# Kernel optimization log

Hardware: AMD Instinct MI355X
Metric: run time of the kernel (lower is better)

The kernel has to match this reference:

```python
import jax, jax.numpy as jnp
import numpy as np
from jax import lax

D_MODEL = 512
D_STATE = 32
D_CONV = 4
D_INNER = 2 * D_MODEL
DT_RANK = (D_MODEL + 15) // 16  # 32
B_SZ, L = 8, 1024
EPS = 1e-12


def _mamba_params(key, pfx):
    ks = jax.random.split(key, 6)
    s = 0.02
    p = {}
    p[pfx + '_in_w'] = jax.random.normal(ks[0], (2 * D_INNER, D_MODEL)) * s
    p[pfx + '_conv_w'] = jax.random.normal(ks[1], (D_INNER, D_CONV)) * s
    p[pfx + '_conv_b'] = jnp.zeros((D_INNER,))
    p[pfx + '_xproj_w'] = jax.random.normal(ks[2], (DT_RANK + 2 * D_STATE, D_INNER)) * s
    p[pfx + '_dt_w'] = jax.random.normal(ks[3], (D_INNER, DT_RANK)) * s
    p[pfx + '_dt_b'] = jax.random.uniform(ks[4], (D_INNER,), minval=-4.0, maxval=-2.0)
    p[pfx + '_A_log'] = jnp.log(jnp.broadcast_to(jnp.arange(1, D_STATE + 1, dtype=jnp.float32), (D_INNER, D_STATE)))
    p[pfx + '_D'] = jnp.ones((D_INNER,))
    p[pfx + '_out_w'] = jax.random.normal(ks[5], (D_MODEL, D_INNER)) * s
    return p


def setup_inputs() -> dict:
    key = jax.random.key(0)
    ks = jax.random.split(key, 10)
    inp = {
        'hidden_states': jax.random.normal(ks[0], (B_SZ, L, D_MODEL)),
        'lengths': jax.random.randint(ks[1], (B_SZ,), 1, L + 1, dtype=jnp.int32),
    }
    inp.update(_mamba_params(ks[2], 'f'))
    inp.update(_mamba_params(ks[3], 'b'))
    s = 0.02
    inp['proj_w'] = jax.random.normal(ks[4], (1, 2)) * 0.5 + 0.5
    inp['proj_b'] = jnp.zeros((1,))
    inp['ln_g'] = jnp.ones((D_MODEL,))
    inp['ln_b'] = jnp.zeros((D_MODEL,))
    inp['ffn_w1'] = jax.random.normal(ks[5], (4 * D_MODEL, D_MODEL)) * s
    inp['ffn_b1'] = jnp.zeros((4 * D_MODEL,))
    inp['ffn_w2'] = jax.random.normal(ks[6], (D_MODEL, 4 * D_MODEL)) * s
    inp['ffn_b2'] = jnp.zeros((D_MODEL,))
    inp['ffn_ln_g'] = jnp.ones((D_MODEL,))
    inp['ffn_ln_b'] = jnp.zeros((D_MODEL,))
    return inp


def _layernorm(x, g, b):
    mu = jnp.mean(x, -1, keepdims=True)
    var = jnp.mean(jnp.square(x - mu), -1, keepdims=True)
    return (x - mu) * lax.rsqrt(var + EPS) * g + b


def _selective_scan(delta, Bm, Cm, u, A, D):
    # delta,u: (B,L,Di); Bm,Cm: (B,L,N); A: (Di,N); D: (Di,)
    def step(h, inp):
        d_t, B_t, C_t, u_t = inp
        dA = jnp.exp(d_t[..., None] * A)                 # (B,Di,N)
        h = dA * h + (d_t * u_t)[..., None] * B_t[:, None, :]
        y = jnp.einsum('bdn,bn->bd', h, C_t)
        return h, y
    h0 = jnp.zeros((u.shape[0], A.shape[0], A.shape[1]), u.dtype)
    xs = (delta.transpose(1, 0, 2), Bm.transpose(1, 0, 2),
          Cm.transpose(1, 0, 2), u.transpose(1, 0, 2))
    _, ys = lax.scan(step, h0, xs)
    return ys.transpose(1, 0, 2) + u * D


def _mamba(x, in_w, conv_w, conv_b, xproj_w, dt_w, dt_b, A_log, Dp, out_w):
    xz = jnp.einsum('bld,ed->ble', x, in_w)              # (B,L,2Di)
    x_in, z = jnp.split(xz, 2, axis=-1)
    # causal depthwise conv1d
    xc = jnp.pad(x_in.transpose(0, 2, 1), ((0, 0), (0, 0), (D_CONV - 1, 0)))
    xc = lax.conv_general_dilated(xc, conv_w[:, None, :], (1,), 'VALID',
                                  dimension_numbers=('NCH', 'OIH', 'NCH'),
                                  feature_group_count=D_INNER)
    xc = jax.nn.silu(xc + conv_b[None, :, None]).transpose(0, 2, 1)  # (B,L,Di)
    x_dbl = jnp.einsum('bld,ed->ble', xc, xproj_w)
    dt, Bm, Cm = jnp.split(x_dbl, [DT_RANK, DT_RANK + D_STATE], axis=-1)
    delta = jax.nn.softplus(jnp.einsum('blr,dr->bld', dt, dt_w) + dt_b)
    A = -jnp.exp(A_log)
    y = _selective_scan(delta, Bm, Cm, xc, A, Dp)
    y = y * jax.nn.silu(z)
    return jnp.einsum('bld,ed->ble', y, out_w)


def reference(hidden_states, lengths,
              f_in_w, f_conv_w, f_conv_b, f_xproj_w, f_dt_w, f_dt_b, f_A_log, f_D, f_out_w,
              b_in_w, b_conv_w, b_conv_b, b_xproj_w, b_dt_w, b_dt_b, b_A_log, b_D, b_out_w,
              proj_w, proj_b, ln_g, ln_b,
              ffn_w1, ffn_b1, ffn_w2, ffn_b2, ffn_ln_g, ffn_ln_b):
    x = hidden_states
    hf = _mamba(x, f_in_w, f_conv_w, f_conv_b, f_xproj_w, f_dt_w, f_dt_b, f_A_log, f_D, f_out_w)
    hb = _mamba(jnp.flip(x, 1), b_in_w, b_conv_w, b_conv_b, b_xproj_w, b_dt_w, b_dt_b, b_A_log, b_D, b_out_w)
    hb = jnp.flip(hb, 1)
    # Linear(2,1) over stacked [hf,hb] on last axis
    out = hf * proj_w[0, 0] + hb * proj_w[0, 1] + proj_b[0]
    out1 = _layernorm(out + x, ln_g, ln_b)  # dropout = identity (eval)
    h = jax.nn.gelu(jnp.einsum('bld,ed->ble', out1, ffn_w1) + ffn_b1, approximate=False)
    h = jnp.einsum('ble,de->bld', h, ffn_w2) + ffn_b2
    return _layernorm(h + out1, ffn_ln_g, ffn_ln_b)
```

## Files before the change

### kernel.cpp

```cpp
#include <hip/hip_runtime.h>
#include <hip/hip_bf16.h>
#include <hip/hip_fp16.h>
#include <math.h>

typedef __hip_bfloat16 bf16;
typedef __attribute__((ext_vector_type(8))) short bfrag;
typedef __attribute__((ext_vector_type(4))) float ffrag;
typedef __attribute__((ext_vector_type(4))) float f4;
typedef __attribute__((ext_vector_type(4))) short sh4;

#define BSZ    8
#define LSEQ   1024
#define DMODEL 512
#define DINNER 1024
#define DSTATE 32
#define DTRANK 32
#define MROWS  (BSZ * LSEQ)

__device__ __forceinline__ float bf2f(bf16 v) { return __bfloat162float(v); }
__device__ __forceinline__ float s2f(short s) {
    union { unsigned u; float f; } c; c.u = ((unsigned)(unsigned short)s) << 16; return c.f;
}
__device__ __forceinline__ short f2s(float v) {
    union { bf16 b; short s; } u; u.b = __float2bfloat16(v); return u.s;
}
__device__ __forceinline__ void stC(float* p, size_t i, float v) { p[i] = v; }
__device__ __forceinline__ void stC(bf16* p, size_t i, float v) { p[i] = __float2bfloat16(v); }
__device__ __forceinline__ float fsigmoid(float x) {
    return __builtin_amdgcn_rcpf(1.f + __expf(-x));
}
__device__ __forceinline__ float fexp2(float x) { return __builtin_amdgcn_exp2f(x); }

__device__ __forceinline__ float dload(const void* p, size_t i, int f) {
    if (f == 1) return ((const float*)p)[i];
    if (f == 2) return __half2float(((const __half*)p)[i]);
    if (f == 3) return (float)((const double*)p)[i];
    return bf2f(((const bf16*)p)[i]);
}

enum { ACT_NONE = 0, ACT_SOFTPLUS = 1, ACT_GELU = 2 };

__global__ void resolve_kernel(const void* a8, const void* d9, const void* d22,
                               const void* s0, const void* s1, int* flags)
{
    if (blockIdx.x != 0) return;
    const int lane = threadIdx.x;
    const int cand[4] = {1, 0, 2, 3};
    int fw = -1;
    for (int ci = 0; ci < 4 && fw < 0; ++ci) {
        int f = cand[ci];
        bool ok = true;
        if (lane < 48) {
            float e = logf((float)((lane & 31) + 1));
            float v = dload(a8, lane, f);
            ok = (v == v) && fabsf(v - e) <= 0.02f * e + 0.02f;
        } else if (lane < 56) {
            int k = lane - 48;
            ok = fabsf(dload(d9, k, f) - 1.f) <= 0.01f &&
                 fabsf(dload(d22, k, f) - 1.f) <= 0.01f;
        }
        if (__all(ok)) fw = f;
    }
    int fx = -1, xs = -1;
    for (int si = 0; si < 2 && fx < 0; ++si) {
        const void* p = (si == 0) ? s0 : s1;
        for (int ci = 0; ci < 4 && fx < 0; ++ci) {
            int f = cand[ci];
            bool ok = true;
            float s = 0.f, s2 = 0.f;
            for (int k = lane; k < 256; k += 64) {
                float v = dload(p, k, f);
                ok = ok && (v == v) && fabsf(v) < 16.f;
                s += v; s2 += v * v;
            }
            int allok = __all(ok);
            for (int m = 1; m < 64; m <<= 1) {
                s += __shfl_xor(s, m); s2 += __shfl_xor(s2, m);
            }
            if (allok) {
                float mu = s * (1.f / 256.f);
                float var = s2 * (1.f / 256.f) - mu * mu;
                if (var > 0.25f && var < 4.f) { fx = f; xs = si; }
            }
        }
    }
    if (lane == 0) {
        flags[0] = (fw < 0) ? 1 : fw;
        flags[1] = (fx < 0) ? 1 : fx;
        flags[2] = (xs < 0) ? 0 : xs;
        flags[3] = (fw == 1 && fx == 1) ? 1 : 0;
    }
}

__global__ __launch_bounds__(256) void cvt_x_kernel(const void* x0, const void* x1,
                                                    bf16* __restrict__ dst,
                                                    const int* __restrict__ flags)
{
    const void* x = flags[2] ? x1 : x0;
    const int fx = flags[1];
    int i = blockIdx.x * 256 + threadIdx.x;
    if (fx == 1) {
        f4 v = ((const f4*)x)[i];
        sh4 o;
#pragma unroll
        for (int j = 0; j < 4; ++j) o[j] = f2s(v[j]);
        ((sh4*)dst)[i] = o;
    } else {
#pragma unroll
        for (int j = 0; j < 4; ++j)
            dst[(size_t)i * 4 + j] = __float2bfloat16(dload(x, (size_t)i * 4 + j, fx));
    }
}

__global__ __launch_bounds__(256) void cvt3_kernel(
    const float* __restrict__ s0, bf16* __restrict__ d0, int n0,
    const float* __restrict__ s1, bf16* __restrict__ d1, int n1,
    const float* __restrict__ s2, bf16* __restrict__ d2, int n2)
{
    int i = blockIdx.x * 256 + threadIdx.x;
    const float* s; bf16* d; int off;
    if (i < n0) { s = s0; d = d0; off = i; }
    else if (i < n0 + n1) { s = s1; d = d1; off = i - n0; }
    else if (i < n0 + n1 + n2) { s = s2; d = d2; off = i - n0 - n1; }
    else return;
    f4 v = ((const f4*)s)[off];
    sh4 o;
#pragma unroll
    for (int j = 0; j < 4; ++j) o[j] = f2s(v[j]);
    ((sh4*)d)[off] = o;
}

__global__ __launch_bounds__(256) void transpose_kernel(
    const bf16* __restrict__ src, bf16* __restrict__ dst, int R, int D)
{
    __shared__ short t[64][72];
    const int r0 = blockIdx.x * 64, d0 = blockIdx.y * 64;
    const int tr = threadIdx.x >> 3;
    const int tc = (threadIdx.x & 7) * 8;
#pragma unroll
    for (int h = 0; h < 2; ++h) {
        int d = tr + h * 32;
        bfrag v = *(const bfrag*)&src[(size_t)(d0 + d) * R + r0 + tc];
#pragma unroll
        for (int j = 0; j < 8; ++j) t[tc + j][d] = v[j];
    }
    __syncthreads();
#pragma unroll
    for (int h = 0; h < 2; ++h) {
        int r = tr + h * 32;
        bfrag v = *(const bfrag*)&t[r][tc];
        *(bfrag*)&dst[(size_t)(r0 + r) * D + d0 + tc] = v;
    }
}

__global__ __launch_bounds__(256) void transpose_f32_kernel(
    const float* __restrict__ src, float* __restrict__ dst, int R)
{
    __shared__ float t[64][68];
    const int m0 = blockIdx.x * 64;
    const int tr = threadIdx.x >> 2;
    const int tc = (threadIdx.x & 3) * 16;
#pragma unroll
    for (int j = 0; j < 4; ++j) {
        f4 v = *(const f4*)&src[(size_t)tr * R + m0 + tc + j * 4];
#pragma unroll
        for (int e = 0; e < 4; ++e) t[tc + j * 4 + e][tr] = v[e];
    }
    __syncthreads();
#pragma unroll
    for (int j = 0; j < 4; ++j) {
        f4 v = *(const f4*)&t[tr][tc + j * 4];
        *(f4*)&dst[(size_t)(m0 + tr) * 64 + tc + j * 4] = v;
    }
}

__device__ __forceinline__ void glds16(const bf16* g, short* l)
{
    __builtin_amdgcn_global_load_lds(
        (const __attribute__((address_space(1))) void*)g,
        (__attribute__((address_space(3))) void*)l,
        16, 0, 0);
}

template <int FLIPB, int ACT, typename CT>
__global__ __launch_bounds__(256) void bgemm_kernel(
    const bf16* __restrict__ A, int lda,
    const bf16* __restrict__ B, int ldb,
    const float* __restrict__ bias,
    CT* __restrict__ C, int ldc, int K)
{
    __shared__ __align__(16) short As[2][128 * 32];
    __shared__ __align__(16) short Bs[2][128 * 32];
    const int tid = threadIdx.x;
    const int bm = blockIdx.y * 128, bn = blockIdx.x * 128;
    const int lane = tid & 63, w = tid >> 6;

    const int srow = lane >> 2;
    const int skc  = (lane & 3) << 3;
    const int arow0 = bm + w * 32 + srow;
    int brow0 = bn + w * 32 + srow;
    int brow1 = brow0 + 16;
    if (FLIPB) {
        brow0 = (brow0 & ~(LSEQ - 1)) + (LSEQ - 1 - (brow0 & (LSEQ - 1)));
        brow1 = (brow1 & ~(LSEQ - 1)) + (LSEQ - 1 - (brow1 & (LSEQ - 1)));
    }
    const bf16* ga0 = A + (size_t)arow0 * lda + skc;
    const bf16* ga1 = ga0 + (size_t)16 * lda;
    const bf16* gb0 = B + (size_t)brow0 * ldb + skc;
    const bf16* gb1 = B + (size_t)brow1 * ldb + skc;
    const int lA0 = (w * 32) * 32, lA1 = (w * 32 + 16) * 32;

    const int wm = (w & 1) << 6, wn = (w >> 1) << 6;
    const int lm = lane & 15, quad = lane >> 4;

    ffrag acc[4][4];
#pragma unroll
    for (int i = 0; i < 4; ++i)
#pragma unroll
        for (int j = 0; j < 4; ++j)
#pragma unroll
            for (int e = 0; e < 4; ++e) acc[i][j][e] = 0.f;

    glds16(ga0, &As[0][lA0]);
    glds16(ga1, &As[0][lA1]);
    glds16(gb0, &Bs[0][lA0]);
    glds16(gb1, &Bs[0][lA1]);
    __syncthreads();

    int cur = 0;
    for (int k0 = 0; k0 < K; k0 += 32) {
        if (k0 + 32 < K) {
            glds16(ga0 + k0 + 32, &As[cur ^ 1][lA0]);
            glds16(ga1 + k0 + 32, &As[cur ^ 1][lA1]);
            glds16(gb0 + k0 + 32, &Bs[cur ^ 1][lA0]);
            glds16(gb1 + k0 + 32, &Bs[cur ^ 1][lA1]);
        }
        bfrag af[4], bfv[4];
#pragma unroll
        for (int ti = 0; ti < 4; ++ti)
            af[ti] = *(const bfrag*)&As[cur][(wm + ti * 16 + lm) * 32 + quad * 8];
#pragma unroll
        for (int tj = 0; tj < 4; ++tj)
            bfv[tj] = *(const bfrag*)&Bs[cur][(wn + tj * 16 + lm) * 32 + quad * 8];
#pragma unroll
        for (int ti = 0; ti < 4; ++ti)
#pragma unroll
            for (int tj = 0; tj < 4; ++tj)
                acc[ti][tj] = __builtin_amdgcn_mfma_f32_16x16x32_bf16(
                    af[ti], bfv[tj], acc[ti][tj], 0, 0, 0);
        __syncthreads();
        cur ^= 1;
    }

#pragma unroll
    for (int tj = 0; tj < 4; ++tj) {
        int col = bn + wn + tj * 16 + lm;
        float bcv = bias ? bias[col] : 0.f;
#pragma unroll
        for (int ti = 0; ti < 4; ++ti) {
#pragma unroll
            for (int r2 = 0; r2 < 4; ++r2) {
                int rowg = bm + wm + ti * 16 + quad * 4 + r2;
                float v = acc[ti][tj][r2] + bcv;
                if (ACT == ACT_GELU) v = 0.5f * v * (1.f + erff(v * 0.70710678118654752f));
                stC(C, (size_t)rowg * ldc + col, v);
            }
        }
    }
}

template <int ACT, typename CT>
__global__ __launch_bounds__(256) void bgemm64_kernel(
    const bf16* __restrict__ A, int lda,
    const bf16* __restrict__ B, int ldb,
    const float* __restrict__ bias,
    CT* __restrict__ C, int ldc, int M, int K)
{
    __shared__ __align__(16) short As[2][128 * 64];
    __shared__ __align__(16) short Bs[2][64 * 64];
    const int tid = threadIdx.x;
    const int bm = blockIdx.y * 128, bn = blockIdx.x * 64;
    const int lane = tid & 63, w = tid >> 6;

    const int lr = lane >> 3;
    const int sc = ((lane & 7) ^ lr) << 3;

    const bf16* ga[4];
#pragma unroll
    for (int a = 0; a < 4; ++a) {
        int ar = bm + w * 32 + a * 8 + lr;
        if (ar >= M) ar = M - 1;
        ga[a] = A + (size_t)ar * lda + sc;
    }
    const bf16* gb[2];
#pragma unroll
    for (int a = 0; a < 2; ++a) {
        int br = bn + w * 16 + a * 8 + lr;
        gb[a] = B + (size_t)br * ldb + sc;
    }
    const int lA = (w * 32) * 64, lB = (w * 16) * 64;

    const int wm = (w & 1) << 6, wn = (w >> 1) << 5;
    const int lm = lane & 15, quad = lane >> 4;

    ffrag acc[4][2];
#pragma unroll
    for (int i = 0; i < 4; ++i)
#pragma unroll
        for (int j = 0; j < 2; ++j)
#pragma unroll
            for (int e = 0; e < 4; ++e) acc[i][j][e] = 0.f;

#pragma unroll
    for (int a = 0; a < 4; ++a) glds16(ga[a], &As[0][lA + a * 8 * 64]);
#pragma unroll
    for (int a = 0; a < 2; ++a) glds16(gb[a], &Bs[0][lB + a * 8 * 64]);
    __syncthreads();

    int cur = 0;
    for (int k0 = 0; k0 < K; k0 += 64) {
        if (k0 + 64 < K) {
#pragma unroll
            for (int a = 0; a < 4; ++a) glds16(ga[a] + k0 + 64, &As[cur ^ 1][lA + a * 8 * 64]);
#pragma unroll
            for (int a = 0; a < 2; ++a) glds16(gb[a] + k0 + 64, &Bs[cur ^ 1][lB + a * 8 * 64]);
        }
        bfrag af[2][4], bfv[2][2];
#pragma unroll
        for (int kk = 0; kk < 2; ++kk) {
#pragma unroll
            for (int ti = 0; ti < 4; ++ti) {
                int row = wm + ti * 16 + lm;
                int c = kk * 4 + quad;
                af[kk][ti] = *(const bfrag*)&As[cur][row * 64 + ((c ^ (row & 7)) << 3)];
            }
#pragma unroll
            for (int tj = 0; tj < 2; ++tj) {
                int row = wn + tj * 16 + lm;
                int c = kk * 4 + quad;
                bfv[kk][tj] = *(const bfrag*)&Bs[cur][row * 64 + ((c ^ (row & 7)) << 3)];
            }
        }
#pragma unroll
        for (int kk = 0; kk < 2; ++kk)
#pragma unroll
            for (int ti = 0; ti < 4; ++ti)
#pragma unroll
                for (int tj = 0; tj < 2; ++tj)
                    acc[ti][tj] = __builtin_amdgcn_mfma_f32_16x16x32_bf16(
                        af[kk][ti], bfv[kk][tj], acc[ti][tj], 0, 0, 0);
        __syncthreads();
        cur ^= 1;
    }

#pragma unroll
    for (int tj = 0; tj < 2; ++tj) {
        int col = bn + wn + tj * 16 + lm;
        float bcv = bias ? bias[col] : 0.f;
#pragma unroll
        for (int ti = 0; ti < 4; ++ti) {
#pragma unroll
            for (int r2 = 0; r2 < 4; ++r2) {
                int rowg = bm + wm + ti * 16 + quad * 4 + r2;
                if (rowg < M) {
                    float v = acc[ti][tj][r2] + bcv;
                    if (ACT == ACT_GELU) v = 0.5f * v * (1.f + erff(v * 0.70710678118654752f));
                    stC(C, (size_t)rowg * ldc + col, v);
                }
            }
        }
    }
}

__global__ __launch_bounds__(256) void dt_kernel(
    const float* __restrict__ xdT,
    const float* __restrict__ dt_w,
    const float* __restrict__ dt_b,
    bf16* __restrict__ delta_T)
{
    const int m = blockIdx.x * 256 + threadIdx.x;
    const int d0 = blockIdx.y * 64;
    float v[32];
#pragma unroll
    for (int r = 0; r < 32; ++r) v[r] = xdT[(size_t)r * MROWS + m];
    for (int d = d0; d < d0 + 64; ++d) {
        float acc = dt_b[d];
#pragma unroll
        for (int r = 0; r < 32; ++r) acc = fmaf(dt_w[d * 32 + r], v[r], acc);
        acc = (acc > 20.f) ? acc : log1pf(__expf(acc));
        delta_T[(size_t)d * MROWS + m] = __float2bfloat16(acc);
    }
}

__global__ __launch_bounds__(256) void conv_silu_kernel(
    const bf16* __restrict__ xin_T,
    const void* __restrict__ cw,
    const void* __restrict__ cb,
    bf16* __restrict__ u_T,
    const int* __restrict__ flags)
{
    const int fw = flags[0];
    int blk = blockIdx.x;
    int chunk = blk & 3;
    int db = blk >> 2;
    int b = db & 7;
    int d = db >> 3;
    int l = chunk * 256 + threadIdx.x;
    size_t base = (size_t)d * MROWS + b * LSEQ;
    float w0 = dload(cw, d * 4 + 0, fw), w1 = dload(cw, d * 4 + 1, fw);
    float w2 = dload(cw, d * 4 + 2, fw), w3 = dload(cw, d * 4 + 3, fw);
    float acc = dload(cb, d, fw);
    if (l >= 3) acc += bf2f(xin_T[base + l - 3]) * w0;
    if (l >= 2) acc += bf2f(xin_T[base + l - 2]) * w1;
    if (l >= 1) acc += bf2f(xin_T[base + l - 1]) * w2;
    acc += bf2f(xin_T[base + l]) * w3;
    u_T[base + l] = __float2bfloat16(acc * fsigmoid(acc));
}

#define SCH 8
struct ScanBuf { float dl[SCH], uv[SCH], Bv[SCH], Cv[SCH]; float zsc, usc; };

__device__ __forceinline__ void scan_load(ScanBuf& s,
    const bf16* __restrict__ dT, const bf16* __restrict__ uT,
    const bf16* __restrict__ zT, const float* __restrict__ xm,
    size_t lb, size_t mb, int n)
{
    bfrag dv = *(const bfrag*)&dT[lb];
    bfrag uv = *(const bfrag*)&uT[lb];
#pragma unroll
    for (int j = 0; j < SCH; ++j) { s.dl[j] = s2f(dv[j]); s.uv[j] = s2f(uv[j]); }
    s.zsc = bf2f(zT[lb + (n & 7)]);
    s.usc = bf2f(uT[lb + (n & 7)]);
#pragma unroll
    for (int j = 0; j < SCH; ++j) {
        s.Bv[j] = xm[(mb + j) * 64 + n];
        s.Cv[j] = xm[(mb + j) * 64 + 32 + n];
    }
}

__device__ __forceinline__ void scan_compute(const ScanBuf& s, float& h,
    float Ad2, float Dd, bf16* __restrict__ yT, size_t lb,
    bool b0, bool b1, bool b2, bool wr)
{
    float p[SCH];
#pragma unroll
    for (int j = 0; j < SCH; ++j) {
        float dlv = s.dl[j];
        h = fexp2(dlv * Ad2) * h + dlv * s.uv[j] * s.Bv[j];
        p[j] = h * s.Cv[j];
    }
    float q[4];
#pragma unroll
    for (int jj = 0; jj < 4; ++jj) {
        float keep = b0 ? p[2 * jj + 1] : p[2 * jj];
        float send = b0 ? p[2 * jj] : p[2 * jj + 1];
        q[jj] = keep + __shfl_xor(send, 1);
    }
    float r0 = (b1 ? q[1] : q[0]) + __shfl_xor(b1 ? q[0] : q[1], 2);
    float r1 = (b1 ? q[3] : q[2]) + __shfl_xor(b1 ? q[2] : q[3], 2);
    float t = (b2 ? r1 : r0) + __shfl_xor(b2 ? r0 : r1, 4);
    t += __shfl_xor(t, 8);
    t += __shfl_xor(t, 16);
    if (wr) {
        float y = t + s.usc * Dd;
        float g = s.zsc;
        y *= g * fsigmoid(g);
        yT[lb + (threadIdx.x & 7)] = __float2bfloat16(y);
    }
}

__global__ __launch_bounds__(256) void scan_kernel(
    const bf16* __restrict__ delta_T,
    bf16* __restrict__ u_T,
    const bf16* __restrict__ z_T,
    const float* __restrict__ xdbl_m,
    const void* __restrict__ A_log,
    const void* __restrict__ Dp,
    const int* __restrict__ flags)
{
    const int fw = flags[0];
    const int tid = threadIdx.x;
    const int n = tid & 31;
    const int dloc = tid >> 5;
    const int gd = blockIdx.x * 8 + dloc;
    const int b = gd >> 10;
    const int d = gd & (DINNER - 1);
    const bool b0 = n & 1, b1 = n & 2, b2 = n & 4;
    const bool wr = (n < 8);

    const float Ad2 = -__expf(dload(A_log, d * DSTATE + n, fw)) * 1.44269504088896341f;
    const float Dd = dload(Dp, d, fw);
    const size_t lbase = (size_t)d * MROWS + b * LSEQ;
    const size_t mbase = (size_t)b * LSEQ;
    float h = 0.f;

    ScanBuf bufA, bufB;
    scan_load(bufA, delta_T, u_T, z_T, xdbl_m, lbase, mbase, n);
    for (int c0 = 0; c0 < LSEQ / SCH; c0 += 2) {
        scan_load(bufB, delta_T, u_T, z_T, xdbl_m,
                  lbase + (size_t)(c0 + 1) * SCH, mbase + (size_t)(c0 + 1) * SCH, n);
        scan_compute(bufA, h, Ad2, Dd, u_T, lbase + (size_t)c0 * SCH, b0, b1, b2, wr);
        if (c0 + 2 < LSEQ / SCH)
            scan_load(bufA, delta_T, u_T, z_T, xdbl_m,
                      lbase + (size_t)(c0 + 2) * SCH, mbase + (size_t)(c0 + 2) * SCH, n);
        scan_compute(bufB, h, Ad2, Dd, u_T, lbase + (size_t)(c0 + 1) * SCH, b0, b1, b2, wr);
    }
}

__global__ __launch_bounds__(256) void combine_ln_kernel(
    const bf16* __restrict__ hf, const bf16* __restrict__ hb,
    const void* __restrict__ x0, const void* __restrict__ x1,
    const void* __restrict__ pw, const void* __restrict__ pb,
    const void* __restrict__ g, const void* __restrict__ be,
    bf16* __restrict__ out1,
    const int* __restrict__ flags)
{
    const int fw = flags[0];
    const int fx = flags[1];
    const void* x = flags[2] ? x1 : x0;
    int row = blockIdx.x;
    int b = row >> 10, l = row & (LSEQ - 1);
    int rrow = (b << 10) + (LSEQ - 1 - l);
    float pw0 = dload(pw, 0, fw), pw1 = dload(pw, 1, fw), pbv = dload(pb, 0, fw);
    __shared__ float red[2][4];
    float v[2], s = 0.f, s2 = 0.f;
#pragma unroll
    for (int i = 0; i < 2; ++i) {
        int c = threadIdx.x + i * 256;
        float val = bf2f(hf[(size_t)row * DMODEL + c]) * pw0
                  + bf2f(hb[(size_t)rrow * DMODEL + c]) * pw1
                  + pbv + dload(x, (size_t)row * DMODEL + c, fx);
        v[i] = val; s += val; s2 += val * val;
    }
    for (int m = 1; m < 64; m <<= 1) { s += __shfl_xor(s, m); s2 += __shfl_xor(s2, m); }
    int w = threadIdx.x >> 6;
    if ((threadIdx.x & 63) == 0) { red[0][w] = s; red[1][w] = s2; }
    __syncthreads();
    s = red[0][0] + red[0][1] + red[0][2] + red[0][3];
    s2 = red[1][0] + red[1][1] + red[1][2] + red[1][3];
    float mu = s * (1.f / DMODEL);
    float var = s2 * (1.f / DMODEL) - mu * mu;
    float r = rsqrtf(fmaxf(var, 0.f) + 1e-12f);
#pragma unroll
    for (int i = 0; i < 2; ++i) {
        int c = threadIdx.x + i * 256;
        float val = (v[i] - mu) * r * dload(g, c, fw) + dload(be, c, fw);
        out1[(size_t)row * DMODEL + c] = __float2bfloat16(val);
    }
}

__global__ __launch_bounds__(256) void final_ln_kernel(
    const float* __restrict__ out2, const bf16* __restrict__ out1,
    const void* __restrict__ g, const void* __restrict__ be,
    float* __restrict__ out,
    const int* __restrict__ flags)
{
    const int fw = flags[0];
    const int valid = flags[3];
    int row = blockIdx.x;
    __shared__ float red[2][4];
    float v[2], s = 0.f, s2 = 0.f;
#pragma unroll
    for (int i = 0; i < 2; ++i) {
        int c = threadIdx.x + i * 256;
        float val = out2[(size_t)row * DMODEL + c] + bf2f(out1[(size_t)row * DMODEL + c]);
        v[i] = val; s += val; s2 += val * val;
    }
    for (int m = 1; m < 64; m <<= 1) { s += __shfl_xor(s, m); s2 += __shfl_xor(s2, m); }
    int w = threadIdx.x >> 6;
    if ((threadIdx.x & 63) == 0) { red[0][w] = s; red[1][w] = s2; }
    __syncthreads();
    s = red[0][0] + red[0][1] + red[0][2] + red[0][3];
    s2 = red[1][0] + red[1][1] + red[1][2] + red[1][3];
    float mu = s * (1.f / DMODEL);
    float var = s2 * (1.f / DMODEL) - mu * mu;
    float r = rsqrtf(fmaxf(var, 0.f) + 1e-12f);
#pragma unroll
    for (int i = 0; i < 2; ++i) {
        int c = threadIdx.x + i * 256;
        float val = (v[i] - mu) * r * dload(g, c, fw) + dload(be, c, fw);
        out[(size_t)row * DMODEL + c] = valid ? val : 0.f;
    }
}

extern "C" void kernel_launch(void* const* d_in, const int* in_sizes, int n_in,
                              void* d_out, int out_size, void* d_ws, size_t ws_size,
                              hipStream_t stream)
{
    const void* x0 = d_in[0];
    const void* x1 = d_in[1];
    const void* proj_w   = d_in[20];
    const void* proj_b   = d_in[21];
    const void* ln_g     = d_in[22];
    const void* ln_b     = d_in[23];
    const float* ffn_w1  = (const float*)d_in[24];
    const float* ffn_b1  = (const float*)d_in[25];
    const float* ffn_w2  = (const float*)d_in[26];
    const float* ffn_b2  = (const float*)d_in[27];
    const void* ffn_ln_g = d_in[28];
    const void* ffn_ln_b = d_in[29];

    char* wsb = (char*)d_ws;
    char* ob  = (char*)d_out;
    bf16*  xin_T   = (bf16*)(wsb + 0);
    bf16*  z_T     = (bf16*)(wsb + (16u << 20));
    bf16*  uy_T    = (bf16*)(wsb + (32u << 20));
    bf16*  u_rm    = (bf16*)(wsb + 0);
    bf16*  delta_T = (bf16*)(wsb + 0);
    bf16*  y_rm    = (bf16*)(wsb + 0);
    float* xdT     = (float*)(wsb + (48u << 20));
    bf16*  in_w_bf = (bf16*)(wsb + (51u << 20));
    float* xdbl_m  = (float*)(wsb + (51u << 20));
    bf16*  xp_w_bf = (bf16*)(wsb + (53u << 20));
    bf16*  o_w_bf  = (bf16*)(wsb + (54u << 20));
    bf16*  hf      = (bf16*)d_out;
    bf16*  hb      = (bf16*)d_out + (size_t)MROWS * DMODEL;
    bf16*  xbf     = (bf16*)(ob + (8u << 20));
    bf16*  w1bf    = (bf16*)(ob + 0);
    bf16*  w2bf    = (bf16*)(ob + (2u << 20));
    bf16*  out1    = (bf16*)(wsb + 0);
    bf16*  ffn_h   = (bf16*)(wsb + (8u << 20));
    float* out2    = (float*)(wsb + (40u << 20));
    int*   flags   = (int*)(wsb + (56u << 20));

    dim3 blk(256);

    resolve_kernel<<<dim3(1), dim3(64), 0, stream>>>(
        d_in[8], d_in[9], d_in[22], x0, x1, flags);
    cvt_x_kernel<<<dim3(4096), blk, 0, stream>>>(x0, x1, xbf, flags);

    for (int dir = 0; dir < 2; ++dir) {
        int pb0 = 2 + dir * 9;
        const float* in_w    = (const float*)d_in[pb0 + 0];
        const void*  conv_w  = d_in[pb0 + 1];
        const void*  conv_b  = d_in[pb0 + 2];
        const float* xproj_w = (const float*)d_in[pb0 + 3];
        const float* dt_w    = (const float*)d_in[pb0 + 4];
        const float* dt_b    = (const float*)d_in[pb0 + 5];
        const void*  A_log   = d_in[pb0 + 6];
        const void*  Dp      = d_in[pb0 + 7];
        const float* out_w   = (const float*)d_in[pb0 + 8];
        bf16* hout = (dir == 0) ? hf : hb;

        cvt3_kernel<<<dim3(1632), blk, 0, stream>>>(
            in_w, in_w_bf, (2048 * 512) / 4,
            xproj_w, xp_w_bf, (96 * 1024) / 4,
            out_w, o_w_bf, (512 * 1024) / 4);

        if (dir == 0)
            bgemm_kernel<0, ACT_NONE, bf16><<<dim3(64, 16), blk, 0, stream>>>(
                in_w_bf, DMODEL, xbf, DMODEL, nullptr, xin_T, MROWS, DMODEL);
        else
            bgemm_kernel<1, ACT_NONE, bf16><<<dim3(64, 16), blk, 0, stream>>>(
                in_w_bf, DMODEL, xbf, DMODEL, nullptr, xin_T, MROWS, DMODEL);

        conv_silu_kernel<<<dim3(DINNER * BSZ * 4), blk, 0, stream>>>(
            xin_T, conv_w, conv_b, uy_T, flags);
        transpose_kernel<<<dim3(128, 16), blk, 0, stream>>>(uy_T, u_rm, MROWS, DINNER);
        bgemm64_kernel<ACT_NONE, float><<<dim3(128, 1), blk, 0, stream>>>(
            xp_w_bf, DINNER, u_rm, DINNER, nullptr, xdT, MROWS, 96, DINNER);
        transpose_f32_kernel<<<dim3(128), blk, 0, stream>>>(
            xdT + (size_t)32 * MROWS, xdbl_m, MROWS);
        dt_kernel<<<dim3(32, 16), blk, 0, stream>>>(xdT, dt_w, dt_b, delta_T);
        scan_kernel<<<dim3((BSZ * DINNER) / 8), blk, 0, stream>>>(
            delta_T, uy_T, z_T, xdbl_m, A_log, Dp, flags);
        transpose_kernel<<<dim3(128, 16), blk, 0, stream>>>(uy_T, y_rm, MROWS, DINNER);
        bgemm64_kernel<ACT_NONE, bf16><<<dim3(8, 64), blk, 0, stream>>>(
            y_rm, DINNER, o_w_bf, DINNER, nullptr, hout, DMODEL, MROWS, DINNER);
    }

    combine_ln_kernel<<<dim3(MROWS), blk, 0, stream>>>(
        hf, hb, x0, x1, proj_w, proj_b, ln_g, ln_b, out1, flags);
    cvt3_kernel<<<dim3(2048), blk, 0, stream>>>(
        ffn_w1, w1bf, (2048 * 512) / 4,
        ffn_w2, w2bf, (512 * 2048) / 4,
        nullptr, nullptr, 0);
    bgemm_kernel<0, ACT_GELU, bf16><<<dim3(16, 64), blk, 0, stream>>>(
        out1, DMODEL, w1bf, DMODEL, ffn_b1, ffn_h, 2048, DMODEL);
    bgemm64_kernel<ACT_NONE, float><<<dim3(8, 64), blk, 0, stream>>>(
        ffn_h, 2048, w2bf, 2048, ffn_b2, out2, DMODEL, MROWS, 2048);
    final_ln_kernel<<<dim3(MROWS), blk, 0, stream>>>(
        out2, out1, ffn_ln_g, ffn_ln_b, (float*)d_out, flags);
}
```

Before: 869.3 us.

## Fuse x_proj B/C transpose into GEMM epilogue with scan-friendly blocked layout

The x_proj GEMM epilogue now writes the dt rows as before but scatters the B and C rows directly into a blocked layout ([m/8][64][8]). This removes the separate f32 transpose kernel from each direction. The scan kernel then loads its 8 B and 8 C values per chunk as two float4 vectors each instead of 16 strided scalar loads. The cost is scattered, less coalesced stores in the GEMM epilogue.

Result: faster. 849.8 us (-2.2%).

```diff
diff --git a/kernel.cpp b/kernel.cpp
--- a/kernel.cpp
+++ b/kernel.cpp
@@ -153,27 +153,6 @@
     }
 }
 
-__global__ __launch_bounds__(256) void transpose_f32_kernel(
-    const float* __restrict__ src, float* __restrict__ dst, int R)
-{
-    __shared__ float t[64][68];
-    const int m0 = blockIdx.x * 64;
-    const int tr = threadIdx.x >> 2;
-    const int tc = (threadIdx.x & 3) * 16;
-#pragma unroll
-    for (int j = 0; j < 4; ++j) {
-        f4 v = *(const f4*)&src[(size_t)tr * R + m0 + tc + j * 4];
-#pragma unroll
-        for (int e = 0; e < 4; ++e) t[tc + j * 4 + e][tr] = v[e];
-    }
-    __syncthreads();
-#pragma unroll
-    for (int j = 0; j < 4; ++j) {
-        f4 v = *(const f4*)&t[tr][tc + j * 4];
-        *(f4*)&dst[(size_t)(m0 + tr) * 64 + tc + j * 4] = v;
-    }
-}
-
 __device__ __forceinline__ void glds16(const bf16* g, short* l)
 {
     __builtin_amdgcn_global_load_lds(
@@ -269,12 +248,14 @@
     }
 }
 
-template <int ACT, typename CT>
+template <int ACT, int XPROJ, typename CT>
 __global__ __launch_bounds__(256) void bgemm64_kernel(
     const bf16* __restrict__ A, int lda,
     const bf16* __restrict__ B, int ldb,
     const float* __restrict__ bias,
-    CT* __restrict__ C, int ldc, int M, int K)
+    CT* __restrict__ C, int ldc,
+    float* __restrict__ C2,
+    int M, int K)
 {
     __shared__ __align__(16) short As[2][128 * 64];
     __shared__ __align__(16) short Bs[2][64 * 64];
@@ -362,7 +343,13 @@
 #pragma unroll
             for (int r2 = 0; r2 < 4; ++r2) {
                 int rowg = bm + wm + ti * 16 + quad * 4 + r2;
-                if (rowg < M) {
+                if (XPROJ) {
+                    float v = acc[ti][tj][r2];
+                    if (rowg < 32)
+                        ((float*)C)[(size_t)rowg * ldc + col] = v;
+                    else if (rowg < 96)
+                        C2[(((size_t)col >> 3) * 64 + (rowg - 32)) * 8 + (col & 7)] = v;
+                } else if (rowg < M) {
                     float v = acc[ti][tj][r2] + bcv;
                     if (ACT == ACT_GELU) v = 0.5f * v * (1.f + erff(v * 0.70710678118654752f));
                     stC(C, (size_t)rowg * ldc + col, v);
@@ -423,7 +410,7 @@
 __device__ __forceinline__ void scan_load(ScanBuf& s,
     const bf16* __restrict__ dT, const bf16* __restrict__ uT,
     const bf16* __restrict__ zT, const float* __restrict__ xm,
-    size_t lb, size_t mb, int n)
+    size_t lb, int coff, int n)
 {
     bfrag dv = *(const bfrag*)&dT[lb];
     bfrag uv = *(const bfrag*)&uT[lb];
@@ -431,10 +418,16 @@
     for (int j = 0; j < SCH; ++j) { s.dl[j] = s2f(dv[j]); s.uv[j] = s2f(uv[j]); }
     s.zsc = bf2f(zT[lb + (n & 7)]);
     s.usc = bf2f(uT[lb + (n & 7)]);
-#pragma unroll
-    for (int j = 0; j < SCH; ++j) {
-        s.Bv[j] = xm[(mb + j) * 64 + n];
-        s.Cv[j] = xm[(mb + j) * 64 + 32 + n];
+    const float* bp = xm + coff + n * 8;
+    f4 b0 = *(const f4*)bp;
+    f4 b1 = *(const f4*)(bp + 4);
+    const float* cp = bp + 256;
+    f4 c0 = *(const f4*)cp;
+    f4 c1 = *(const f4*)(cp + 4);
+#pragma unroll
+    for (int j = 0; j < 4; ++j) {
+        s.Bv[j] = b0[j]; s.Bv[4 + j] = b1[j];
+        s.Cv[j] = c0[j]; s.Cv[4 + j] = c1[j];
     }
 }
 
@@ -491,18 +484,18 @@
     const float Ad2 = -__expf(dload(A_log, d * DSTATE + n, fw)) * 1.44269504088896341f;
     const float Dd = dload(Dp, d, fw);
     const size_t lbase = (size_t)d * MROWS + b * LSEQ;
-    const size_t mbase = (size_t)b * LSEQ;
+    const float* xmb = xdbl_m + ((size_t)b * LSEQ >> 3) * 512;
     float h = 0.f;
 
     ScanBuf bufA, bufB;
-    scan_load(bufA, delta_T, u_T, z_T, xdbl_m, lbase, mbase, n);
+    scan_load(bufA, delta_T, u_T, z_T, xmb, lbase, 0, n);
     for (int c0 = 0; c0 < LSEQ / SCH; c0 += 2) {
-        scan_load(bufB, delta_T, u_T, z_T, xdbl_m,
-                  lbase + (size_t)(c0 + 1) * SCH, mbase + (size_t)(c0 + 1) * SCH, n);
+        scan_load(bufB, delta_T, u_T, z_T, xmb,
+                  lbase + (size_t)(c0 + 1) * SCH, (c0 + 1) * 512, n);
         scan_compute(bufA, h, Ad2, Dd, u_T, lbase + (size_t)c0 * SCH, b0, b1, b2, wr);
         if (c0 + 2 < LSEQ / SCH)
-            scan_load(bufA, delta_T, u_T, z_T, xdbl_m,
-                      lbase + (size_t)(c0 + 2) * SCH, mbase + (size_t)(c0 + 2) * SCH, n);
+            scan_load(bufA, delta_T, u_T, z_T, xmb,
+                      lbase + (size_t)(c0 + 2) * SCH, (c0 + 2) * 512, n);
         scan_compute(bufB, h, Ad2, Dd, u_T, lbase + (size_t)(c0 + 1) * SCH, b0, b1, b2, wr);
     }
 }
@@ -657,16 +650,14 @@
         conv_silu_kernel<<<dim3(DINNER * BSZ * 4), blk, 0, stream>>>(
             xin_T, conv_w, conv_b, uy_T, flags);
         transpose_kernel<<<dim3(128, 16), blk, 0, stream>>>(uy_T, u_rm, MROWS, DINNER);
-        bgemm64_kernel<ACT_NONE, float><<<dim3(128, 1), blk, 0, stream>>>(
-            xp_w_bf, DINNER, u_rm, DINNER, nullptr, xdT, MROWS, 96, DINNER);
-        transpose_f32_kernel<<<dim3(128), blk, 0, stream>>>(
-            xdT + (size_t)32 * MROWS, xdbl_m, MROWS);
+        bgemm64_kernel<ACT_NONE, 1, float><<<dim3(128, 1), blk, 0, stream>>>(
+            xp_w_bf, DINNER, u_rm, DINNER, nullptr, xdT, MROWS, xdbl_m, 96, DINNER);
         dt_kernel<<<dim3(32, 16), blk, 0, stream>>>(xdT, dt_w, dt_b, delta_T);
         scan_kernel<<<dim3((BSZ * DINNER) / 8), blk, 0, stream>>>(
             delta_T, uy_T, z_T, xdbl_m, A_log, Dp, flags);
         transpose_kernel<<<dim3(128, 16), blk, 0, stream>>>(uy_T, y_rm, MROWS, DINNER);
-        bgemm64_kernel<ACT_NONE, bf16><<<dim3(8, 64), blk, 0, stream>>>(
-            y_rm, DINNER, o_w_bf, DINNER, nullptr, hout, DMODEL, MROWS, DINNER);
+        bgemm64_kernel<ACT_NONE, 0, bf16><<<dim3(8, 64), blk, 0, stream>>>(
+            y_rm, DINNER, o_w_bf, DINNER, nullptr, hout, DMODEL, nullptr, MROWS, DINNER);
     }
 
     combine_ln_kernel<<<dim3(MROWS), blk, 0, stream>>>(
@@ -677,8 +668,8 @@
         nullptr, nullptr, 0);
     bgemm_kernel<0, ACT_GELU, bf16><<<dim3(16, 64), blk, 0, stream>>>(
         out1, DMODEL, w1bf, DMODEL, ffn_b1, ffn_h, 2048, DMODEL);
-    bgemm64_kernel<ACT_NONE, float><<<dim3(8, 64), blk, 0, stream>>>(
-        ffn_h, 2048, w2bf, 2048, ffn_b2, out2, DMODEL, MROWS, 2048);
+    bgemm64_kernel<ACT_NONE, 0, float><<<dim3(8, 64), blk, 0, stream>>>(
+        ffn_h, 2048, w2bf, 2048, ffn_b2, out2, DMODEL, nullptr, MROWS, 2048);
     final_ln_kernel<<<dim3(MROWS), blk, 0, stream>>>(
         out2, out1, ffn_ln_g, ffn_ln_b, (float*)d_out, flags);
 }
```
